# Kernel tuning notes

Measured on AMD Instinct MI355X. Metric: run time of the kernel, lower is better.

The kernel has to match this reference:

```python
import jax, jax.numpy as jnp
import numpy as np

V, H, L, B = 32000, 512, 128, 8
PAD = 0


def setup_inputs() -> dict:
    key = jax.random.key(0)
    ks = jax.random.split(key, 20)
    s = 0.02
    inp = {
        "input_": jax.random.randint(ks[0], (B, L), 0, V),
        "encoder_inputs": jax.random.randint(ks[1], (B, L), 0, V),
        "encoder_hidden": jax.random.normal(ks[2], (1, B, H), jnp.float32),
        "encoder_outputs": jax.random.normal(ks[3], (B, L, H), jnp.float32),
        "emb_table": jax.random.normal(ks[4], (V, H), jnp.float32) * s,
        "attn_W": jax.random.normal(ks[5], (L, 2 * H), jnp.float32) * s,
        "attn_b": jnp.zeros((L,), jnp.float32),
        "comb_W": jax.random.normal(ks[6], (H, 2 * H), jnp.float32) * s,
        "comb_b": jnp.zeros((H,), jnp.float32),
        "gru_Wih": jax.random.normal(ks[7], (3 * H, H), jnp.float32) * s,
        "gru_Whh": jax.random.normal(ks[8], (3 * H, H), jnp.float32) * s,
        "gru_bih": jnp.zeros((3 * H,), jnp.float32),
        "gru_bhh": jnp.zeros((3 * H,), jnp.float32),
        "out_W": jax.random.normal(ks[9], (V, H), jnp.float32) * s,
        "out_b": jnp.zeros((V,), jnp.float32),
        "dogen_W": jax.random.normal(ks[10], (1, 3 * H), jnp.float32) * s,
        "dogen_b": jnp.zeros((1,), jnp.float32),
        "copy_W": jax.random.normal(ks[11], (1, 2 * H), jnp.float32) * s,
        "copy_b": jnp.zeros((1,), jnp.float32),
    }
    return inp


def _gru(x, h0, Wih, Whh, bih, bhh):
    # x: [B,L,H] batch_first; h0: [B,H]. PyTorch GRU gate math.
    def step(h, x_t):
        gi = x_t @ Wih.T + bih  # [B,3H]
        gh = h @ Whh.T + bhh
        i_r, i_z, i_n = jnp.split(gi, 3, axis=-1)
        h_r, h_z, h_n = jnp.split(gh, 3, axis=-1)
        r = jax.nn.sigmoid(i_r + h_r)
        z = jax.nn.sigmoid(i_z + h_z)
        n = jnp.tanh(i_n + r * h_n)
        h_new = (1.0 - z) * n + z * h
        return h_new, h_new
    _, ys = jax.lax.scan(step, h0, jnp.swapaxes(x, 0, 1))  # ys: [L,B,H]
    return jnp.swapaxes(ys, 0, 1)


def reference(input_, encoder_inputs, encoder_hidden, encoder_outputs, emb_table,
              attn_W, attn_b, comb_W, comb_b, gru_Wih, gru_Whh, gru_bih, gru_bhh,
              out_W, out_b, dogen_W, dogen_b, copy_W, copy_b):
    # Dropout is identity (eval mode).
    embedded = emb_table[input_]  # [B,L,H]
    h0 = encoder_hidden[0]  # [B,H]
    hid_exp = jnp.broadcast_to(h0[:, None, :], embedded.shape)
    attn_logits = jnp.concatenate([embedded, hid_exp], axis=2) @ attn_W.T + attn_b  # [B,L,L]
    attn_weights = jax.nn.softmax(attn_logits, axis=1)  # softmax over dim=1 (as in torch code)
    attn_applied = jnp.einsum('bij,bjh->bih', attn_weights, encoder_outputs)
    x = jnp.concatenate([embedded, attn_applied], axis=2) @ comb_W.T + comb_b
    x = jax.nn.relu(x)
    output = _gru(x, h0, gru_Wih, gru_Whh, gru_bih, gru_bhh)  # [B,L,H]
    generation_dist = jax.nn.softmax(output @ out_W.T + out_b, axis=2)  # [B,L,V]
    # get_alpha: copy_weight_proj is rank-1 over concat([e_states, d_states]);
    # compute without materializing the [B,L,L,2H] cross product.
    w_e, w_d = copy_W[0, :H], copy_W[0, H:]
    e_part = encoder_outputs @ w_e  # [B,L] (indexed by j)
    d_part = output @ w_d           # [B,L] (indexed by i)
    logits = d_part[:, :, None] + e_part[:, None, :] + copy_b[0]  # [B,L_dec,L_enc]
    pad_pen = jnp.where(encoder_inputs == PAD, -1000.0, 0.0)
    logits = logits + pad_pen[:, None, :]
    alphas = jax.nn.softmax(logits, axis=2)
    context = jnp.einsum('bij,bjh->bih', alphas, encoder_outputs)
    # scatter_add: index repeats encoder_inputs[b,i] along j, so all alpha mass
    # of row (b,i) lands at vocab id encoder_inputs[b,i].
    row_sum = alphas.sum(axis=2)  # [B,L]
    b_idx = jnp.arange(B)[:, None]
    i_idx = jnp.arange(L)[None, :]
    copy_dist = jnp.zeros((B, L, V), generation_dist.dtype).at[b_idx, i_idx, encoder_inputs].add(row_sum)
    mix = jax.nn.sigmoid(jnp.concatenate([output, context, embedded], axis=2) @ dogen_W.T + dogen_b)  # [B,L,1]
    prob = generation_dist * mix + copy_dist * (1.0 - mix)
    return prob, attn_weights
```

## Files before the change

### kernel.cpp

```cpp
#include <hip/hip_runtime.h>
#include <cstdint>

#define VDIM 32000
#define HDIM 512
#define LDIM 128
#define BDIM 8
#define MROWS 1024
#define H2 1024
#define H3 1536
#define GRU_WGS 32
#define HSTEP 8192

typedef __bf16 bf16x8 __attribute__((ext_vector_type(8)));
typedef float f32x4 __attribute__((ext_vector_type(4)));

#define AS1 __attribute__((address_space(1)))
#define AS3 __attribute__((address_space(3)))

__device__ __forceinline__ unsigned short f2b(float x) {
  unsigned u = __builtin_bit_cast(unsigned, x);
  u += 0x7fffu + ((u >> 16) & 1u);
  return (unsigned short)(u >> 16);
}

__device__ __forceinline__ float wredS(float v) {
#pragma unroll
  for (int o = 32; o > 0; o >>= 1) v += __shfl_xor(v, o);
  return v;
}
__device__ __forceinline__ float wredM(float v) {
#pragma unroll
  for (int o = 32; o > 0; o >>= 1) v = fmaxf(v, __shfl_xor(v, o));
  return v;
}

__device__ __forceinline__ void gl_lds16(const void* g, void* l) {
  __builtin_amdgcn_global_load_lds((AS1 void*)const_cast<void*>(g), (AS3 void*)l, 16, 0, 0);
}

__global__ void cvt_kernel(const float* __restrict__ src, unsigned short* __restrict__ dst, int n4) {
  int i = blockIdx.x * 256 + threadIdx.x;
  if (i < n4) {
    float4 v = ((const float4*)src)[i];
    unsigned r0 = (unsigned)f2b(v.x) | ((unsigned)f2b(v.y) << 16);
    unsigned r1 = (unsigned)f2b(v.z) | ((unsigned)f2b(v.w) << 16);
    uint2 r; r.x = r0; r.y = r1;
    *(uint2*)(dst + (size_t)i * 4) = r;
  }
}

__global__ void hzero_kernel(unsigned short* __restrict__ hbufbf) {
  size_t i = (size_t)blockIdx.x * 256 + threadIdx.x;
  uint4 z = {0, 0, 0, 0};
  size_t n8 = (size_t)129 * HSTEP / 8;
  if (i < n8) ((uint4*)hbufbf)[i] = z;
}

__global__ void init_kernel(const float* __restrict__ h0, unsigned short* __restrict__ hbufbf,
                            float* __restrict__ rowsum, int* __restrict__ cnt) {
  int tid = threadIdx.x;
  for (int i = tid; i < BDIM * HDIM; i += 256) {
    int b = i >> 9, k = i & 511;
    hbufbf[b * 512 + k] = f2b(h0[i]);
  }
  for (int i = tid; i < MROWS; i += 256) rowsum[i] = 0.f;
  for (int i = tid; i < 160; i += 256) cnt[i] = (i == 0) ? GRU_WGS : 0;
}

__global__ void embed_kernel(const int* __restrict__ input_, const float* __restrict__ emb,
                             float* __restrict__ emb_f, unsigned short* __restrict__ A4) {
  int m = blockIdx.x, tid = threadIdx.x;
  int tok = input_[m];
  const float* src = emb + (size_t)tok * HDIM;
  for (int k = tid; k < HDIM; k += 256) {
    float v = src[k];
    emb_f[(size_t)m * HDIM + k] = v;
    A4[(size_t)m * H2 + k] = f2b(v);
  }
}

__global__ void attn_kernel(const float* __restrict__ emb_f, const float* __restrict__ h0,
                            const float* __restrict__ attn_W, const float* __restrict__ attn_b,
                            float* __restrict__ attn_out) {
  int j = blockIdx.x, b = blockIdx.y, tid = threadIdx.x;
  int wid = tid >> 6;
  __shared__ float wj[H2];
  __shared__ float red[2];
  for (int k = tid; k < H2; k += 128) wj[k] = attn_W[(size_t)j * H2 + k];
  __syncthreads();
  float hp = 0.f;
  for (int k = tid * 4; k < tid * 4 + 4; ++k) hp += h0[b * HDIM + k] * wj[HDIM + k];
  hp = wredS(hp);
  if ((tid & 63) == 0) red[wid] = hp;
  __syncthreads();
  float hdot = red[0] + red[1];
  __syncthreads();

  int i = tid;
  const float* er = emb_f + ((size_t)(b * LDIM + i)) * HDIM;
  float acc = 0.f;
  for (int k = 0; k < HDIM; k += 4) {
    float4 e = *(const float4*)(er + k);
    acc += e.x * wj[k] + e.y * wj[k + 1] + e.z * wj[k + 2] + e.w * wj[k + 3];
  }
  float l = acc + hdot + attn_b[j];
  float mx = wredM(l);
  if ((tid & 63) == 0) red[wid] = mx;
  __syncthreads();
  mx = fmaxf(red[0], red[1]);
  __syncthreads();
  float e = __expf(l - mx);
  float s = wredS(e);
  if ((tid & 63) == 0) red[wid] = s;
  __syncthreads();
  s = red[0] + red[1];
  attn_out[(size_t)b * (LDIM * LDIM) + (size_t)i * LDIM + j] = e / s;
}

__global__ void einsum_kernel(const float* __restrict__ w, const float* __restrict__ enc,
                              float* __restrict__ outF, unsigned short* __restrict__ outBf, int mode) {
  int i = blockIdx.x, b = blockIdx.y, tid = threadIdx.x;
  __shared__ float wr[LDIM];
  if (tid < LDIM) wr[tid] = w[((size_t)(b * LDIM + i)) * LDIM + tid];
  __syncthreads();
  float a0 = 0.f, a1 = 0.f;
  const float* eb = enc + (size_t)b * LDIM * HDIM;
  for (int jj = 0; jj < LDIM; ++jj) {
    float wv = wr[jj];
    const float* er = eb + (size_t)jj * HDIM;
    a0 += wv * er[tid];
    a1 += wv * er[tid + 256];
  }
  if (mode == 0) {
    size_t base = ((size_t)(b * LDIM + i)) * H2 + HDIM;
    outBf[base + tid] = f2b(a0);
    outBf[base + tid + 256] = f2b(a1);
  } else {
    size_t base = ((size_t)(b * LDIM + i)) * HDIM;
    outF[base + tid] = a0;
    outF[base + tid + 256] = a1;
  }
}

__global__ __launch_bounds__(256) void gemm_bt(const unsigned short* __restrict__ A,
                                               const unsigned short* __restrict__ Bw, int N, int K,
                                               const float* __restrict__ bias, int mode,
                                               float* __restrict__ outF,
                                               unsigned short* __restrict__ outBf,
                                               float* __restrict__ rowsum) {
  __shared__ unsigned short sA[4096];
  __shared__ unsigned short sB[4096];
  int tid = threadIdx.x;
  int lane = tid & 63, w = tid >> 6;
  int wm = w >> 1, wn = w & 1;
  int ln15 = lane & 15, q = lane >> 4;
  int m0 = blockIdx.y * 128, n0 = blockIdx.x * 128;
  f32x4 acc[4][4] = {};
  int rowA = tid >> 2;
  int colK = (tid & 3) * 8;
  for (int kt = 0; kt < K; kt += 32) {
    __syncthreads();
    const unsigned short* ga0 = A + (size_t)(m0 + rowA) * K + kt + colK;
    const unsigned short* ga1 = A + (size_t)(m0 + 64 + rowA) * K + kt + colK;
    const unsigned short* gb0 = Bw + (size_t)(n0 + rowA) * K + kt + colK;
    const unsigned short* gb1 = Bw + (size_t)(n0 + 64 + rowA) * K + kt + colK;
    gl_lds16(ga0, sA + w * 512);
    gl_lds16(ga1, sA + 2048 + w * 512);
    gl_lds16(gb0, sB + w * 512);
    gl_lds16(gb1, sB + 2048 + w * 512);
    __syncthreads();
    bf16x8 af[4], bf[4];
#pragma unroll
    for (int t = 0; t < 4; ++t) {
      af[t] = *(const bf16x8*)(sA + (wm * 64 + t * 16 + ln15) * 32 + q * 8);
      bf[t] = *(const bf16x8*)(sB + (wn * 64 + t * 16 + ln15) * 32 + q * 8);
    }
#pragma unroll
    for (int ti = 0; ti < 4; ++ti)
#pragma unroll
      for (int tj = 0; tj < 4; ++tj)
        acc[ti][tj] = __builtin_amdgcn_mfma_f32_16x16x32_bf16(af[ti], bf[tj], acc[ti][tj], 0, 0, 0);
  }
#pragma unroll
  for (int ti = 0; ti < 4; ++ti) {
#pragma unroll
    for (int reg = 0; reg < 4; ++reg) {
      int m = m0 + wm * 64 + ti * 16 + q * 4 + reg;
      float s = 0.f;
#pragma unroll
      for (int tj = 0; tj < 4; ++tj) {
        int n = n0 + wn * 64 + tj * 16 + ln15;
        float c = acc[ti][tj][reg] + bias[n];
        if (mode == 2) {
          float e = __expf(c);
          outF[(size_t)m * N + n] = e;
          s += e;
        } else if (mode == 0) {
          outBf[(size_t)m * N + n] = f2b(fmaxf(c, 0.f));
        } else {
          outF[(size_t)m * N + n] = c;
        }
      }
      if (mode == 2) {
        s += __shfl_xor(s, 1); s += __shfl_xor(s, 2);
        s += __shfl_xor(s, 4); s += __shfl_xor(s, 8);
        if (ln15 == 0) atomicAdd(&rowsum[m], s);
      }
    }
  }
}

__global__ __launch_bounds__(64) void gru_kernel(const float* __restrict__ Whh,
                                                 const float* __restrict__ bhh,
                                                 const float* __restrict__ gi,
                                                 const float* __restrict__ h0,
                                                 unsigned short* __restrict__ hbufbf,
                                                 float* __restrict__ outF,
                                                 unsigned short* __restrict__ Ab,
                                                 int* __restrict__ cnt) {
  __shared__ unsigned short sW[3 * 16 * 64 * 8];
  int g = blockIdx.x, lane = threadIdx.x;
  int ln15 = lane & 15, q = lane >> 4;
  int j = g * 16 + ln15;
#pragma unroll 1
  for (int gate = 0; gate < 3; ++gate) {
#pragma unroll 1
    for (int kk = 0; kk < 16; ++kk) {
      const float* src = Whh + (size_t)(gate * 512 + g * 16 + ln15) * 512 + kk * 32 + q * 8;
      float4 v0 = *(const float4*)src, v1 = *(const float4*)(src + 4);
      unsigned short* dst = sW + (size_t)((gate * 16 + kk) * 64 + lane) * 8;
      dst[0] = f2b(v0.x); dst[1] = f2b(v0.y); dst[2] = f2b(v0.z); dst[3] = f2b(v0.w);
      dst[4] = f2b(v1.x); dst[5] = f2b(v1.y); dst[6] = f2b(v1.z); dst[7] = f2b(v1.w);
    }
  }
  float bh_r = bhh[j], bh_z = bhh[512 + j], bh_n = bhh[1024 + j];
  float hreg[4];
  if (q < 2) {
#pragma unroll
    for (int reg = 0; reg < 4; ++reg) hreg[reg] = h0[(q * 4 + reg) * 512 + j];
  }
  __syncthreads();

  for (int t = 0; t < 128; ++t) {
    float gir[4], giz[4], gin[4];
    if (q < 2) {
#pragma unroll
      for (int reg = 0; reg < 4; ++reg) {
        size_t gib = ((size_t)((q * 4 + reg) * 128 + t)) * H3;
        gir[reg] = gi[gib + j];
        giz[reg] = gi[gib + 512 + j];
        gin[reg] = gi[gib + 1024 + j];
      }
    }
    if (lane == 0) {
      while (__hip_atomic_load(&cnt[t], __ATOMIC_ACQUIRE, __HIP_MEMORY_SCOPE_AGENT) < GRU_WGS)
        __builtin_amdgcn_s_sleep(1);
    }
    __syncthreads();
    const unsigned short* hT = hbufbf + (size_t)t * HSTEP + ln15 * 512 + q * 8;
    bf16x8 aF[16];
#pragma unroll
    for (int kk = 0; kk < 16; ++kk) aF[kk] = *(const bf16x8*)(hT + kk * 32);
    f32x4 ac0 = {}, ac1 = {}, ac2 = {};
#pragma unroll
    for (int kk = 0; kk < 16; ++kk) {
      bf16x8 b0 = *(const bf16x8*)(sW + (size_t)((0 * 16 + kk) * 64 + lane) * 8);
      bf16x8 b1 = *(const bf16x8*)(sW + (size_t)((1 * 16 + kk) * 64 + lane) * 8);
      bf16x8 b2 = *(const bf16x8*)(sW + (size_t)((2 * 16 + kk) * 64 + lane) * 8);
      ac0 = __builtin_amdgcn_mfma_f32_16x16x32_bf16(aF[kk], b0, ac0, 0, 0, 0);
      ac1 = __builtin_amdgcn_mfma_f32_16x16x32_bf16(aF[kk], b1, ac1, 0, 0, 0);
      ac2 = __builtin_amdgcn_mfma_f32_16x16x32_bf16(aF[kk], b2, ac2, 0, 0, 0);
    }
    float hv[4];
    if (q < 2) {
#pragma unroll
      for (int reg = 0; reg < 4; ++reg) {
        int b = q * 4 + reg;
        float rr = 1.f / (1.f + __expf(-(gir[reg] + ac0[reg] + bh_r)));
        float zz = 1.f / (1.f + __expf(-(giz[reg] + ac1[reg] + bh_z)));
        float narg = gin[reg] + rr * (ac2[reg] + bh_n);
        narg = fminf(fmaxf(narg, -20.f), 20.f);
        float te = __expf(2.f * narg);
        float nn = (te - 1.f) / (te + 1.f);
        hv[reg] = (1.f - zz) * nn + zz * hreg[reg];
        hreg[reg] = hv[reg];
        hbufbf[(size_t)(t + 1) * HSTEP + b * 512 + j] = f2b(hv[reg]);
      }
    }
    if (lane == 0)
      __hip_atomic_fetch_add(&cnt[t + 1], 1, __ATOMIC_RELEASE, __HIP_MEMORY_SCOPE_AGENT);
    if (q < 2) {
#pragma unroll
      for (int reg = 0; reg < 4; ++reg) {
        int b = q * 4 + reg;
        size_t orow = ((size_t)b * 128 + t) * 512 + j;
        outF[orow] = hv[reg];
        Ab[orow] = f2b(hv[reg]);
      }
    }
  }
}

__global__ void dots_kernel(const float* __restrict__ enc, const float* __restrict__ outF,
                            const float* __restrict__ copyW, float* __restrict__ epart,
                            float* __restrict__ dpart) {
  int tid = threadIdx.x, lane = tid & 63, wid = tid >> 6;
  int gw = blockIdx.x * 4 + wid;
  for (int row = gw; row < 2048; row += 128) {
    const float* src;
    const float* wv;
    float* dst;
    int r;
    if (row < 1024) { src = enc + (size_t)row * 512; wv = copyW; dst = epart; r = row; }
    else { src = outF + (size_t)(row - 1024) * 512; wv = copyW + 512; dst = dpart; r = row - 1024; }
    float4 s1 = *(const float4*)(src + lane * 8);
    float4 s2 = *(const float4*)(src + lane * 8 + 4);
    float4 w1 = *(const float4*)(wv + lane * 8);
    float4 w2 = *(const float4*)(wv + lane * 8 + 4);
    float p = s1.x * w1.x + s1.y * w1.y + s1.z * w1.z + s1.w * w1.w +
              s2.x * w2.x + s2.y * w2.y + s2.z * w2.z + s2.w * w2.w;
    p = wredS(p);
    if (lane == 0) dst[r] = p;
  }
}

__global__ void alphas_kernel(const float* __restrict__ dpart, const float* __restrict__ epart,
                              const int* __restrict__ enc_in, const float* __restrict__ copy_b,
                              float* __restrict__ alphas) {
  int i = blockIdx.x, b = blockIdx.y, jt = threadIdx.x;
  int wid = jt >> 6;
  __shared__ float red[2];
  float l = dpart[b * 128 + i] + epart[b * 128 + jt] + copy_b[0] +
            (enc_in[b * 128 + jt] == 0 ? -1000.f : 0.f);
  float mx = wredM(l);
  if ((jt & 63) == 0) red[wid] = mx;
  __syncthreads();
  mx = fmaxf(red[0], red[1]);
  __syncthreads();
  float e = __expf(l - mx);
  float s = wredS(e);
  if ((jt & 63) == 0) red[wid] = s;
  __syncthreads();
  s = red[0] + red[1];
  alphas[((size_t)(b * 128 + i)) * 128 + jt] = e / s;
}

__global__ void mix_kernel(const float* __restrict__ outF, const float* __restrict__ ctx,
                           const float* __restrict__ emb_f, const float* __restrict__ dogenW,
                           const float* __restrict__ dogenB, float* __restrict__ mixb) {
  int tid = threadIdx.x, lane = tid & 63, wid = tid >> 6;
  int gw = blockIdx.x * 4 + wid;
  for (int row = gw; row < 1024; row += 64) {
    int k = lane * 8;
    const float* o = outF + (size_t)row * 512;
    const float* c = ctx + (size_t)row * 512;
    const float* e = emb_f + (size_t)row * 512;
    float p = 0.f;
#pragma unroll
    for (int u = 0; u < 8; ++u)
      p += o[k + u] * dogenW[k + u] + c[k + u] * dogenW[512 + k + u] + e[k + u] * dogenW[1024 + k + u];
    p = wredS(p);
    if (lane == 0) mixb[row] = 1.f / (1.f + __expf(-(p + dogenB[0])));
  }
}

__global__ void final_kernel(float* __restrict__ prob, const float* __restrict__ mixb,
                             const float* __restrict__ rowsum, const int* __restrict__ enc_in) {
  int row = blockIdx.y;
  int v = blockIdx.x * 256 + threadIdx.x;
  float mx = mixb[row], rs = rowsum[row];
  size_t idx = (size_t)row * VDIM + v;
  float val = prob[idx] * (mx / rs);
  if (v == enc_in[row]) val += 1.f - mx;
  prob[idx] = val;
}

extern "C" void kernel_launch(void* const* d_in, const int* in_sizes, int n_in, void* d_out,
                              int out_size, void* d_ws, size_t ws_size, hipStream_t stream) {
  const int* input_ = (const int*)d_in[0];
  const int* enc_in = (const int*)d_in[1];
  const float* enc_h = (const float*)d_in[2];
  const float* enc_out = (const float*)d_in[3];
  const float* emb = (const float*)d_in[4];
  const float* attn_W = (const float*)d_in[5];
  const float* attn_b = (const float*)d_in[6];
  const float* comb_W = (const float*)d_in[7];
  const float* comb_b = (const float*)d_in[8];
  const float* Wih = (const float*)d_in[9];
  const float* Whh = (const float*)d_in[10];
  const float* bih = (const float*)d_in[11];
  const float* bhh = (const float*)d_in[12];
  const float* out_W = (const float*)d_in[13];
  const float* out_b = (const float*)d_in[14];
  const float* dogen_W = (const float*)d_in[15];
  const float* dogen_b = (const float*)d_in[16];
  const float* copy_W = (const float*)d_in[17];
  const float* copy_b = (const float*)d_in[18];

  float* prob = (float*)d_out;
  float* attn_out = prob + (size_t)MROWS * VDIM;

  char* ws = (char*)d_ws;
  size_t off = 0;
  auto alloc = [&](size_t bytes) {
    off = (off + 255) & ~(size_t)255;
    void* p = ws + off;
    off += bytes;
    return p;
  };
  unsigned short* outW_bf = (unsigned short*)alloc((size_t)VDIM * HDIM * 2);
  unsigned short* combW_bf = (unsigned short*)alloc((size_t)HDIM * H2 * 2);
  unsigned short* Wih_bf = (unsigned short*)alloc((size_t)H3 * HDIM * 2);
  unsigned short* A4 = (unsigned short*)alloc((size_t)MROWS * H2 * 2);
  unsigned short* xbf = (unsigned short*)alloc((size_t)MROWS * HDIM * 2);
  unsigned short* Ab = (unsigned short*)alloc((size_t)MROWS * HDIM * 2);
  float* emb_f = (float*)alloc((size_t)MROWS * HDIM * 4);
  float* gi = (float*)alloc((size_t)MROWS * H3 * 4);
  float* outF = (float*)alloc((size_t)MROWS * HDIM * 4);
  unsigned short* hbufbf = (unsigned short*)alloc((size_t)129 * HSTEP * 2);
  int* cnt = (int*)alloc(1024);
  float* rowsum = (float*)alloc(4096);
  float* epart = (float*)alloc(4096);
  float* dpart = (float*)alloc(4096);
  float* alphas = (float*)alloc((size_t)MROWS * LDIM * 4);
  float* ctx = (float*)alloc((size_t)MROWS * HDIM * 4);
  float* mixb = (float*)alloc(4096);

  cvt_kernel<<<(VDIM * HDIM / 4 + 255) / 256, 256, 0, stream>>>(out_W, outW_bf, VDIM * HDIM / 4);
  cvt_kernel<<<(HDIM * H2 / 4 + 255) / 256, 256, 0, stream>>>(comb_W, combW_bf, HDIM * H2 / 4);
  cvt_kernel<<<(H3 * HDIM / 4 + 255) / 256, 256, 0, stream>>>(Wih, Wih_bf, H3 * HDIM / 4);
  {
    int n8 = (int)((size_t)129 * HSTEP / 8);
    hzero_kernel<<<(n8 + 255) / 256, 256, 0, stream>>>(hbufbf);
  }
  init_kernel<<<1, 256, 0, stream>>>(enc_h, hbufbf, rowsum, cnt);
  embed_kernel<<<MROWS, 256, 0, stream>>>(input_, emb, emb_f, A4);
  attn_kernel<<<dim3(LDIM, BDIM), 128, 0, stream>>>(emb_f, enc_h, attn_W, attn_b, attn_out);
  einsum_kernel<<<dim3(LDIM, BDIM), 256, 0, stream>>>(attn_out, enc_out, nullptr, A4, 0);
  gemm_bt<<<dim3(4, 8), 256, 0, stream>>>(A4, combW_bf, HDIM, H2, comb_b, 0, nullptr, xbf, nullptr);
  gemm_bt<<<dim3(12, 8), 256, 0, stream>>>(xbf, Wih_bf, H3, HDIM, bih, 1, gi, nullptr, nullptr);
  gru_kernel<<<GRU_WGS, 64, 0, stream>>>(Whh, bhh, gi, enc_h, hbufbf, outF, Ab, cnt);
  gemm_bt<<<dim3(VDIM / 128, 8), 256, 0, stream>>>(Ab, outW_bf, VDIM, HDIM, out_b, 2, prob, nullptr, rowsum);
  dots_kernel<<<32, 256, 0, stream>>>(enc_out, outF, copy_W, epart, dpart);
  alphas_kernel<<<dim3(LDIM, BDIM), 128, 0, stream>>>(dpart, epart, enc_in, copy_b, alphas);
  einsum_kernel<<<dim3(LDIM, BDIM), 256, 0, stream>>>(alphas, enc_out, ctx, nullptr, 1);
  mix_kernel<<<16, 256, 0, stream>>>(outF, ctx, emb_f, dogen_W, dogen_b, mixb);
  final_kernel<<<dim3(VDIM / 256, MROWS), 256, 0, stream>>>(prob, mixb, rowsum, enc_in);
}
```

Before: 1.347 ms.

## Replace GRU step counter with per-workgroup flags and packed stores

The GRU cross-workgroup barrier changes from a single atomic counter per step to one flag per workgroup per step. All 32 lanes poll the flags together with a ballot instead of one lane spinning followed by __syncthreads. The hidden-state buffer stride is halved to 4096, the hzero kernel is removed, and the A fragments for padded rows 8-15 are zero-filled in registers instead of read from memory. Stores are packed in pairs via lane shuffles and the MFMA accumulation is split into two chains. This is meant to cut the per-step synchronization latency and atomic contention on the serial recurrence, at the cost of more polling traffic and a bounded spin loop that could exit early if the flags are never set.

```diff
diff --git a/kernel.cpp b/kernel.cpp
--- a/kernel.cpp
+++ b/kernel.cpp
@@ -9,7 +9,7 @@
 #define H2 1024
 #define H3 1536
 #define GRU_WGS 32
-#define HSTEP 8192
+#define HSTEP 4096
 
 typedef __bf16 bf16x8 __attribute__((ext_vector_type(8)));
 typedef float f32x4 __attribute__((ext_vector_type(4)));
@@ -49,22 +49,15 @@
   }
 }
 
-__global__ void hzero_kernel(unsigned short* __restrict__ hbufbf) {
-  size_t i = (size_t)blockIdx.x * 256 + threadIdx.x;
-  uint4 z = {0, 0, 0, 0};
-  size_t n8 = (size_t)129 * HSTEP / 8;
-  if (i < n8) ((uint4*)hbufbf)[i] = z;
-}
-
 __global__ void init_kernel(const float* __restrict__ h0, unsigned short* __restrict__ hbufbf,
-                            float* __restrict__ rowsum, int* __restrict__ cnt) {
+                            float* __restrict__ rowsum, int* __restrict__ flags) {
   int tid = threadIdx.x;
   for (int i = tid; i < BDIM * HDIM; i += 256) {
     int b = i >> 9, k = i & 511;
     hbufbf[b * 512 + k] = f2b(h0[i]);
   }
   for (int i = tid; i < MROWS; i += 256) rowsum[i] = 0.f;
-  for (int i = tid; i < 160; i += 256) cnt[i] = (i == 0) ? GRU_WGS : 0;
+  for (int i = tid; i < 129 * GRU_WGS; i += 256) flags[i] = (i < GRU_WGS) ? 1 : 0;
 }
 
 __global__ void embed_kernel(const int* __restrict__ input_, const float* __restrict__ emb,
@@ -217,7 +210,7 @@
                                                  unsigned short* __restrict__ hbufbf,
                                                  float* __restrict__ outF,
                                                  unsigned short* __restrict__ Ab,
-                                                 int* __restrict__ cnt) {
+                                                 int* __restrict__ flags) {
   __shared__ unsigned short sW[3 * 16 * 64 * 8];
   int g = blockIdx.x, lane = threadIdx.x;
   int ln15 = lane & 15, q = lane >> 4;
@@ -234,7 +227,7 @@
     }
   }
   float bh_r = bhh[j], bh_z = bhh[512 + j], bh_n = bhh[1024 + j];
-  float hreg[4];
+  float hreg[4] = {0.f, 0.f, 0.f, 0.f};
   if (q < 2) {
 #pragma unroll
     for (int reg = 0; reg < 4; ++reg) hreg[reg] = h0[(q * 4 + reg) * 512 + j];
@@ -252,30 +245,44 @@
         gin[reg] = gi[gib + 1024 + j];
       }
     }
-    if (lane == 0) {
-      while (__hip_atomic_load(&cnt[t], __ATOMIC_ACQUIRE, __HIP_MEMORY_SCOPE_AGENT) < GRU_WGS)
-        __builtin_amdgcn_s_sleep(1);
-    }
-    __syncthreads();
-    const unsigned short* hT = hbufbf + (size_t)t * HSTEP + ln15 * 512 + q * 8;
-    bf16x8 aF[16];
-#pragma unroll
-    for (int kk = 0; kk < 16; ++kk) aF[kk] = *(const bf16x8*)(hT + kk * 32);
-    f32x4 ac0 = {}, ac1 = {}, ac2 = {};
-#pragma unroll
-    for (int kk = 0; kk < 16; ++kk) {
+    const int* fl = flags + t * GRU_WGS;
+    for (int spin = 0; spin < (1 << 20); ++spin) {
+      int f = __hip_atomic_load(&fl[lane & 31], __ATOMIC_RELAXED, __HIP_MEMORY_SCOPE_AGENT);
+      if (__ballot(f != 0) == ~0ull) break;
+      __builtin_amdgcn_s_sleep(1);
+    }
+    __builtin_amdgcn_fence(__ATOMIC_ACQUIRE, "agent");
+    bf16x8 aF[16] = {};
+    if (ln15 < 8) {
+      const unsigned short* hT = hbufbf + (size_t)t * HSTEP + ln15 * 512 + q * 8;
+#pragma unroll
+      for (int kk = 0; kk < 16; ++kk) aF[kk] = *(const bf16x8*)(hT + kk * 32);
+    }
+    f32x4 c0a = {}, c0b = {}, c1a = {}, c1b = {}, c2a = {}, c2b = {};
+#pragma unroll
+    for (int kk = 0; kk < 8; ++kk) {
       bf16x8 b0 = *(const bf16x8*)(sW + (size_t)((0 * 16 + kk) * 64 + lane) * 8);
       bf16x8 b1 = *(const bf16x8*)(sW + (size_t)((1 * 16 + kk) * 64 + lane) * 8);
       bf16x8 b2 = *(const bf16x8*)(sW + (size_t)((2 * 16 + kk) * 64 + lane) * 8);
-      ac0 = __builtin_amdgcn_mfma_f32_16x16x32_bf16(aF[kk], b0, ac0, 0, 0, 0);
-      ac1 = __builtin_amdgcn_mfma_f32_16x16x32_bf16(aF[kk], b1, ac1, 0, 0, 0);
-      ac2 = __builtin_amdgcn_mfma_f32_16x16x32_bf16(aF[kk], b2, ac2, 0, 0, 0);
-    }
-    float hv[4];
+      c0a = __builtin_amdgcn_mfma_f32_16x16x32_bf16(aF[kk], b0, c0a, 0, 0, 0);
+      c1a = __builtin_amdgcn_mfma_f32_16x16x32_bf16(aF[kk], b1, c1a, 0, 0, 0);
+      c2a = __builtin_amdgcn_mfma_f32_16x16x32_bf16(aF[kk], b2, c2a, 0, 0, 0);
+    }
+#pragma unroll
+    for (int kk = 8; kk < 16; ++kk) {
+      bf16x8 b0 = *(const bf16x8*)(sW + (size_t)((0 * 16 + kk) * 64 + lane) * 8);
+      bf16x8 b1 = *(const bf16x8*)(sW + (size_t)((1 * 16 + kk) * 64 + lane) * 8);
+      bf16x8 b2 = *(const bf16x8*)(sW + (size_t)((2 * 16 + kk) * 64 + lane) * 8);
+      c0b = __builtin_amdgcn_mfma_f32_16x16x32_bf16(aF[kk], b0, c0b, 0, 0, 0);
+      c1b = __builtin_amdgcn_mfma_f32_16x16x32_bf16(aF[kk], b1, c1b, 0, 0, 0);
+      c2b = __builtin_amdgcn_mfma_f32_16x16x32_bf16(aF[kk], b2, c2b, 0, 0, 0);
+    }
+    f32x4 ac0 = c0a + c0b, ac1 = c1a + c1b, ac2 = c2a + c2b;
+
+    float hv[4] = {0.f, 0.f, 0.f, 0.f};
     if (q < 2) {
 #pragma unroll
       for (int reg = 0; reg < 4; ++reg) {
-        int b = q * 4 + reg;
         float rr = 1.f / (1.f + __expf(-(gir[reg] + ac0[reg] + bh_r)));
         float zz = 1.f / (1.f + __expf(-(giz[reg] + ac1[reg] + bh_z)));
         float narg = gin[reg] + rr * (ac2[reg] + bh_n);
@@ -284,18 +291,42 @@
         float nn = (te - 1.f) / (te + 1.f);
         hv[reg] = (1.f - zz) * nn + zz * hreg[reg];
         hreg[reg] = hv[reg];
-        hbufbf[(size_t)(t + 1) * HSTEP + b * 512 + j] = f2b(hv[reg]);
-      }
-    }
-    if (lane == 0)
-      __hip_atomic_fetch_add(&cnt[t + 1], 1, __ATOMIC_RELEASE, __HIP_MEMORY_SCOPE_AGENT);
-    if (q < 2) {
+      }
+    }
+    unsigned hb[4];
+    unsigned long long ofp[4];
+#pragma unroll
+    for (int reg = 0; reg < 4; ++reg) {
+      unsigned v = (unsigned)f2b(hv[reg]);
+      unsigned pv = (unsigned)__shfl_xor((int)v, 1);
+      hb[reg] = v | (pv << 16);
+      unsigned fo = __builtin_bit_cast(unsigned, hv[reg]);
+      unsigned fp = (unsigned)__shfl_xor((int)fo, 1);
+      ofp[reg] = (unsigned long long)fo | ((unsigned long long)fp << 32);
+    }
+    bool st = (q < 2) && ((lane & 1) == 0);
+    if (st) {
+      unsigned* hrow = (unsigned*)hbufbf;
 #pragma unroll
       for (int reg = 0; reg < 4; ++reg) {
         int b = q * 4 + reg;
-        size_t orow = ((size_t)b * 128 + t) * 512 + j;
-        outF[orow] = hv[reg];
-        Ab[orow] = f2b(hv[reg]);
+        __hip_atomic_store(&hrow[(size_t)(t + 1) * (HSTEP / 2) + b * 256 + (j >> 1)], hb[reg],
+                           __ATOMIC_RELAXED, __HIP_MEMORY_SCOPE_AGENT);
+      }
+    }
+    __builtin_amdgcn_fence(__ATOMIC_RELEASE, "agent");
+    if (lane == 0)
+      __hip_atomic_store(&flags[(t + 1) * GRU_WGS + g], 1, __ATOMIC_RELAXED,
+                         __HIP_MEMORY_SCOPE_AGENT);
+    if (st) {
+      unsigned* abrow = (unsigned*)Ab;
+      unsigned long long* ofrow = (unsigned long long*)outF;
+#pragma unroll
+      for (int reg = 0; reg < 4; ++reg) {
+        int b = q * 4 + reg;
+        size_t orow2 = ((size_t)b * 128 + t) * 256 + (j >> 1);
+        __hip_atomic_store(&abrow[orow2], hb[reg], __ATOMIC_RELAXED, __HIP_MEMORY_SCOPE_AGENT);
+        __hip_atomic_store(&ofrow[orow2], ofp[reg], __ATOMIC_RELAXED, __HIP_MEMORY_SCOPE_AGENT);
       }
     }
   }
@@ -418,7 +449,7 @@
   float* gi = (float*)alloc((size_t)MROWS * H3 * 4);
   float* outF = (float*)alloc((size_t)MROWS * HDIM * 4);
   unsigned short* hbufbf = (unsigned short*)alloc((size_t)129 * HSTEP * 2);
-  int* cnt = (int*)alloc(1024);
+  int* flags = (int*)alloc(129 * GRU_WGS * 4);
   float* rowsum = (float*)alloc(4096);
   float* epart = (float*)alloc(4096);
   float* dpart = (float*)alloc(4096);
@@ -429,17 +460,13 @@
   cvt_kernel<<<(VDIM * HDIM / 4 + 255) / 256, 256, 0, stream>>>(out_W, outW_bf, VDIM * HDIM / 4);
   cvt_kernel<<<(HDIM * H2 / 4 + 255) / 256, 256, 0, stream>>>(comb_W, combW_bf, HDIM * H2 / 4);
   cvt_kernel<<<(H3 * HDIM / 4 + 255) / 256, 256, 0, stream>>>(Wih, Wih_bf, H3 * HDIM / 4);
-  {
-    int n8 = (int)((size_t)129 * HSTEP / 8);
-    hzero_kernel<<<(n8 + 255) / 256, 256, 0, stream>>>(hbufbf);
-  }
-  init_kernel<<<1, 256, 0, stream>>>(enc_h, hbufbf, rowsum, cnt);
+  init_kernel<<<1, 256, 0, stream>>>(enc_h, hbufbf, rowsum, flags);
   embed_kernel<<<MROWS, 256, 0, stream>>>(input_, emb, emb_f, A4);
   attn_kernel<<<dim3(LDIM, BDIM), 128, 0, stream>>>(emb_f, enc_h, attn_W, attn_b, attn_out);
   einsum_kernel<<<dim3(LDIM, BDIM), 256, 0, stream>>>(attn_out, enc_out, nullptr, A4, 0);
   gemm_bt<<<dim3(4, 8), 256, 0, stream>>>(A4, combW_bf, HDIM, H2, comb_b, 0, nullptr, xbf, nullptr);
   gemm_bt<<<dim3(12, 8), 256, 0, stream>>>(xbf, Wih_bf, H3, HDIM, bih, 1, gi, nullptr, nullptr);
-  gru_kernel<<<GRU_WGS, 64, 0, stream>>>(Whh, bhh, gi, enc_h, hbufbf, outF, Ab, cnt);
+  gru_kernel<<<GRU_WGS, 64, 0, stream>>>(Whh, bhh, gi, enc_h, hbufbf, outF, Ab, flags);
   gemm_bt<<<dim3(VDIM / 128, 8), 256, 0, stream>>>(Ab, outW_bf, VDIM, HDIM, out_b, 2, prob, nullptr, rowsum);
   dots_kernel<<<32, 256, 0, stream>>>(enc_out, outF, copy_W, epart, dpart);
   alphas_kernel<<<dim3(LDIM, BDIM), 128, 0, stream>>>(dpart, epart, enc_in, copy_b, alphas);
```

Result: faster. 1.112 ms (-17.4%).
